# Optimization experiments

Measured on AMD Instinct MI355X. Metric: run time of the kernel, lower is better.

The kernel has to match this reference:

```python
import jax, jax.numpy as jnp
import numpy as np
from jax import lax

B, T, P, I, H = 1024, 100, 50, 96, 1024  # batch, seq_dim, pred_dim, input_dim, hidden_dim


def _gru_cell(x, h, Wih, Whh, bih, bhh):
    # PyTorch GRU gate math. Wih:[3H,in], Whh:[3H,H]
    gi = x @ Wih.T + bih
    gh = h @ Whh.T + bhh
    ir, iz, i_n = jnp.split(gi, 3, axis=-1)
    hr, hz, h_n = jnp.split(gh, 3, axis=-1)
    r = jax.nn.sigmoid(ir + hr)
    z = jax.nn.sigmoid(iz + hz)
    n = jnp.tanh(i_n + r * h_n)
    return (1.0 - z) * n + z * h


def setup_inputs() -> dict:
    key = jax.random.key(0)
    ks = jax.random.split(key, 24)
    s = 1.0 / np.sqrt(H)

    def rn(k, shape):
        return jax.random.normal(k, shape, jnp.float32) * s

    inp = {"x": jax.random.normal(ks[0], (B, T, I), jnp.float32)}
    # encoder nn.GRU: layer 0 input I, layer 1 input H
    inp["enc_Wih0"] = rn(ks[1], (3 * H, I)); inp["enc_Whh0"] = rn(ks[2], (3 * H, H))
    inp["enc_bih0"] = rn(ks[3], (3 * H,));   inp["enc_bhh0"] = rn(ks[4], (3 * H,))
    inp["enc_Wih1"] = rn(ks[5], (3 * H, H)); inp["enc_Whh1"] = rn(ks[6], (3 * H, H))
    inp["enc_bih1"] = rn(ks[7], (3 * H,));   inp["enc_bhh1"] = rn(ks[8], (3 * H,))
    # decoder GRUCells (hidden->hidden)
    inp["dec_Wih0"] = rn(ks[9], (3 * H, H)); inp["dec_Whh0"] = rn(ks[10], (3 * H, H))
    inp["dec_bih0"] = rn(ks[11], (3 * H,));  inp["dec_bhh0"] = rn(ks[12], (3 * H,))
    inp["dec_Wih1"] = rn(ks[13], (3 * H, H)); inp["dec_Whh1"] = rn(ks[14], (3 * H, H))
    inp["dec_bih1"] = rn(ks[15], (3 * H,));  inp["dec_bhh1"] = rn(ks[16], (3 * H,))
    # fc_in: I->H, fc_out: H->I
    inp["fc_in_w"] = rn(ks[17], (H, I)); inp["fc_in_b"] = rn(ks[18], (H,))
    inp["fc_out_w"] = rn(ks[19], (I, H)); inp["fc_out_b"] = rn(ks[20], (I,))
    return inp


def reference(x, enc_Wih0, enc_Whh0, enc_bih0, enc_bhh0,
              enc_Wih1, enc_Whh1, enc_bih1, enc_bhh1,
              dec_Wih0, dec_Whh0, dec_bih0, dec_bhh0,
              dec_Wih1, dec_Whh1, dec_bih1, dec_bhh1,
              fc_in_w, fc_in_b, fc_out_w, fc_out_b):
    b = x.shape[0]
    h0 = jnp.zeros((b, H), x.dtype)
    xs = jnp.transpose(x[:, :P, :], (1, 0, 2))  # [P, B, I]

    def enc0(h, xt):
        h2 = _gru_cell(xt, h, enc_Wih0, enc_Whh0, enc_bih0, enc_bhh0)
        return h2, h2

    h_enc0, seq0 = lax.scan(enc0, h0, xs)

    def enc1(h, xt):
        h2 = _gru_cell(xt, h, enc_Wih1, enc_Whh1, enc_bih1, enc_bhh1)
        return h2, h2

    h_enc1, _ = lax.scan(enc1, h0, seq0)

    def dec_step(carry, _):
        frame, hd0, hd1 = carry
        y = frame @ fc_in_w.T + fc_in_b
        hd0 = _gru_cell(y, hd0, dec_Wih0, dec_Whh0, dec_bih0, dec_bhh0)
        hd1 = _gru_cell(hd0, hd1, dec_Wih1, dec_Whh1, dec_bih1, dec_bhh1)
        frame = hd1 @ fc_out_w.T + fc_out_b + frame
        return (frame, hd0, hd1), frame

    init = (x[:, P - 1, :], h_enc0, h_enc1)
    _, outs = lax.scan(dec_step, init, None, length=T - P)  # [T-P, B, I]
    out = jnp.concatenate([x[:, :P, :], jnp.transpose(outs, (1, 0, 2))], axis=1)
    return out
```

## Files before the change

### kernel.cpp

```cpp
#include <hip/hip_runtime.h>
#include <hip/hip_bf16.h>
#include <stdint.h>

#define Bsz 1024
#define Tt  100
#define Pp  50
#define Ii  96
#define Hh  1024
#define H3  3072

typedef __bf16 bf16x8 __attribute__((ext_vector_type(8)));
typedef float f32x4 __attribute__((ext_vector_type(4)));
typedef __hip_bfloat16 bf16;

__device__ __forceinline__ void llds16(const void* g, void* l) {
    __builtin_amdgcn_global_load_lds(
        (const __attribute__((address_space(1))) void*)g,
        (__attribute__((address_space(3))) void*)l,
        16, 0, 0);
}

__device__ __forceinline__ void swz_decomp(int& bx, int& by, int& bz) {
    int gx = gridDim.x, gy = gridDim.y, gz = gridDim.z;
    int flat = blockIdx.x + gx * (blockIdx.y + gy * blockIdx.z);
    int tot = gx * gy * gz;
    if (!(tot & 7)) {
        int q = tot >> 3;
        flat = (flat & 7) * q + (flat >> 3);
    }
    bx = flat % gx;
    int rest = flat / gx;
    by = rest % gy;
    bz = rest / gy;
}

__global__ void wdesc_k(unsigned long long* slot, const void* A, const void* W,
                        const void* b, void* C, int K, int lda) {
    if (threadIdx.x == 0) {
        slot[0] = (unsigned long long)A;
        slot[1] = (unsigned long long)W;
        slot[2] = (unsigned long long)b;
        slot[3] = (unsigned long long)C;
        slot[4] = (unsigned long long)K;
        slot[5] = (unsigned long long)lda;
    }
}

__global__ void __launch_bounds__(256)
gemm_tab(const unsigned long long* __restrict__ tab, int base, int ndesc,
         const bf16* __restrict__ extraA)
{
    __shared__ bf16 As[128 * 32];
    __shared__ bf16 Ws[128 * 32];
    int flat = blockIdx.x;
    const int tot = ndesc * 192;
    if (!(tot & 7)) {
        int q = tot >> 3;
        flat = (flat & 7) * q + (flat >> 3);
    }
    const int g = flat / 192;
    const int local = flat - g * 192;
    const unsigned long long* dp = tab + (size_t)(base + g) * 8;
    const bf16* A = (const bf16*)dp[0];
    const bf16* W = (const bf16*)dp[1];
    const float* bias = (const float*)dp[2];
    float* C = (float*)dp[3];
    const int K = (int)dp[4];
    const int lda = (int)dp[5];
    if (!A) A = extraA;

    const int tn = (local % 24) * 128;
    const int tm = (local / 24) * 128;

    const int tid = threadIdx.x;
    const int lane = tid & 63;
    const int wid = tid >> 6;
    const int wr = (wid >> 1) * 64;
    const int wc = (wid & 1) * 64;
    const int srow = tid >> 2;
    const int skb = (tid & 3) * 8;

    f32x4 acc[4][4] = {};

    const bf16* ga = A + (size_t)(tm + srow) * lda + skb;
    const bf16* gw = W + (size_t)(tn + srow) * K + skb;
    bf16* lA = &As[srow * 32 + skb];
    bf16* lW = &Ws[srow * 32 + skb];
    const int nk = K >> 5;

    for (int kt = 0; kt < nk; ++kt) {
        llds16(ga, lA);
        llds16(ga + (size_t)64 * lda, lA + 64 * 32);
        llds16(gw, lW);
        llds16(gw + (size_t)64 * K, lW + 64 * 32);
        ga += 32; gw += 32;
        __syncthreads();

        const int fr = lane & 15;
        const int kg = (lane >> 4) * 8;
        bf16x8 af[4], wf[4];
#pragma unroll
        for (int i = 0; i < 4; ++i) {
            af[i] = *(const bf16x8*)&As[(wr + i * 16 + fr) * 32 + kg];
            wf[i] = *(const bf16x8*)&Ws[(wc + i * 16 + fr) * 32 + kg];
        }
#pragma unroll
        for (int mi = 0; mi < 4; ++mi)
#pragma unroll
            for (int ni = 0; ni < 4; ++ni)
                acc[mi][ni] = __builtin_amdgcn_mfma_f32_16x16x32_bf16(
                    af[mi], wf[ni], acc[mi][ni], 0, 0, 0);
        __syncthreads();
    }

    const int fr = lane & 15;
    const int fq = (lane >> 4) * 4;
#pragma unroll
    for (int mi = 0; mi < 4; ++mi)
#pragma unroll
        for (int ni = 0; ni < 4; ++ni) {
            const int col = tn + wc + ni * 16 + fr;
            const float bv = bias[col];
#pragma unroll
            for (int r = 0; r < 4; ++r) {
                const int row = tm + wr + mi * 16 + fq + r;
                C[(size_t)row * H3 + col] = acc[mi][ni][r] + bv;
            }
        }
}

template <bool OUT_BF16>
__global__ void __launch_bounds__(256)
gemm64(const bf16* __restrict__ A, const bf16* __restrict__ W,
       const float* __restrict__ bias, void* __restrict__ Cout,
       int M, int Nreal, int Ktot, int Ks, int lda, int ldc)
{
    __shared__ bf16 As[64 * 32];
    __shared__ bf16 Ws[64 * 32];
    int bx, by, bz;
    swz_decomp(bx, by, bz);
    const int s = bz;
    const float* bs = (s == 0) ? bias : nullptr;
    const int tid = threadIdx.x;
    const int lane = tid & 63;
    const int wid = tid >> 6;
    const int wr = (wid >> 1) * 32;
    const int wc = (wid & 1) * 32;
    const int tm = by * 64;
    const int tn = bx * 64;
    const int srow = tid >> 2;
    const int skb = (tid & 3) * 8;
    const int k0 = s * Ks;

    f32x4 acc[2][2] = {};

    const bf16* ga = A + (size_t)(tm + srow) * lda + k0 + skb;
    const bf16* gw = W + (size_t)(tn + srow) * Ktot + k0 + skb;
    bf16* lA = &As[srow * 32 + skb];
    bf16* lW = &Ws[srow * 32 + skb];
    const int nk = Ks >> 5;

    for (int kt = 0; kt < nk; ++kt) {
        llds16(ga, lA);
        llds16(gw, lW);
        ga += 32; gw += 32;
        __syncthreads();
        const int fr = lane & 15;
        const int kg = (lane >> 4) * 8;
        bf16x8 af[2], wf[2];
#pragma unroll
        for (int i = 0; i < 2; ++i) {
            af[i] = *(const bf16x8*)&As[(wr + i * 16 + fr) * 32 + kg];
            wf[i] = *(const bf16x8*)&Ws[(wc + i * 16 + fr) * 32 + kg];
        }
#pragma unroll
        for (int mi = 0; mi < 2; ++mi)
#pragma unroll
            for (int ni = 0; ni < 2; ++ni)
                acc[mi][ni] = __builtin_amdgcn_mfma_f32_16x16x32_bf16(
                    af[mi], wf[ni], acc[mi][ni], 0, 0, 0);
        __syncthreads();
    }

    float* Cf = (float*)Cout + (size_t)s * M * ldc;
    const int fr = lane & 15;
    const int fq = (lane >> 4) * 4;
#pragma unroll
    for (int mi = 0; mi < 2; ++mi)
#pragma unroll
        for (int ni = 0; ni < 2; ++ni) {
            const int col = tn + wc + ni * 16 + fr;
            if (col < Nreal) {
                const float bv = bs ? bs[col] : 0.f;
#pragma unroll
                for (int r = 0; r < 4; ++r) {
                    const int row = tm + wr + mi * 16 + fq + r;
                    const float v = acc[mi][ni][r] + bv;
                    if constexpr (OUT_BF16)
                        ((bf16*)Cout)[(size_t)row * ldc + col] = __float2bfloat16(v);
                    else
                        Cf[(size_t)row * ldc + col] = v;
                }
            }
        }
}

__global__ void cvt_k(const float* __restrict__ s, bf16* __restrict__ d, int n) {
    int i = blockIdx.x * blockDim.x + threadIdx.x;
    if (i < n) d[i] = __float2bfloat16(s[i]);
}

__global__ void tpose_k(const float* __restrict__ x, bf16* __restrict__ d) {
    int o = blockIdx.x * blockDim.x + threadIdx.x;
    if (o >= Tt * Bsz * Ii) return;
    int i = o % Ii;
    int b = (o / Ii) % Bsz;
    int t = o / (Ii * Bsz);
    d[o] = __float2bfloat16(x[((size_t)b * Tt + t) * Ii + i]);
}

__global__ void tposeFcin_k(const float* __restrict__ w, bf16* __restrict__ d) {
    int o = blockIdx.x * blockDim.x + threadIdx.x;
    if (o >= 128 * Hh) return;
    int r = o >> 10;
    int c = o & (Hh - 1);
    float v = (r < Ii) ? w[(size_t)c * Ii + r] : 0.f;
    d[o] = __float2bfloat16(v);
}

__global__ void __launch_bounds__(256)
bcomb_k(const float* __restrict__ W, const float* __restrict__ v,
        const float* __restrict__ b2, float* __restrict__ o) {
    __shared__ float red[256];
    int n = blockIdx.x;
    float s = 0.f;
    for (int k = threadIdx.x; k < Hh; k += 256)
        s += W[(size_t)n * Hh + k] * v[k];
    red[threadIdx.x] = s;
    __syncthreads();
    for (int w = 128; w > 0; w >>= 1) {
        if (threadIdx.x < w) red[threadIdx.x] += red[threadIdx.x + w];
        __syncthreads();
    }
    if (threadIdx.x == 0) o[n] = red[0] + b2[n];
}

__global__ void prefix_k(const float* __restrict__ x, float* __restrict__ out) {
    int idx = blockIdx.x * blockDim.x + threadIdx.x;
    if (idx >= Bsz * Pp * Ii) return;
    int b = idx / (Pp * Ii);
    int r = idx % (Pp * Ii);
    out[(size_t)b * Tt * Ii + r] = x[(size_t)b * Tt * Ii + r];
}

__global__ void finit_k(const float* __restrict__ x, float* __restrict__ fr,
                        bf16* __restrict__ frb) {
    int idx = blockIdx.x * blockDim.x + threadIdx.x;
    if (idx >= Bsz * Ii) return;
    int b = idx / Ii;
    int i = idx % Ii;
    float v = x[(size_t)b * Tt * Ii + (Pp - 1) * Ii + i];
    fr[idx] = v;
    frb[idx] = __float2bfloat16(v);
}

__global__ void __launch_bounds__(256)
gru_cell_k(const float* __restrict__ giA, const float* __restrict__ giB,
           const float* __restrict__ ghA, const float* __restrict__ ghB,
           float* __restrict__ h, bf16* __restrict__ hb) {
    int idx = blockIdx.x * 256 + threadIdx.x;
    int b = idx >> 8;
    int j = (idx & 255) << 2;
    size_t base = (size_t)b * H3 + j;
    f32x4 ir = *(const f32x4*)(giA + base);
    f32x4 iz = *(const f32x4*)(giA + base + Hh);
    f32x4 in = *(const f32x4*)(giA + base + 2 * Hh);
    if (giB) {
        ir += *(const f32x4*)(giB + base);
        iz += *(const f32x4*)(giB + base + Hh);
        in += *(const f32x4*)(giB + base + 2 * Hh);
    }
    f32x4 hr = *(const f32x4*)(ghA + base);
    f32x4 hz = *(const f32x4*)(ghA + base + Hh);
    f32x4 hn = *(const f32x4*)(ghA + base + 2 * Hh);
    if (ghB) {
        hr += *(const f32x4*)(ghB + base);
        hz += *(const f32x4*)(ghB + base + Hh);
        hn += *(const f32x4*)(ghB + base + 2 * Hh);
    }
    size_t hoff = (size_t)b * Hh + j;
    f32x4 hold = *(const f32x4*)(h + hoff);
    f32x4 hv;
    ushort4 up;
    unsigned short* us = &up.x;
#pragma unroll
    for (int e = 0; e < 4; ++e) {
        float r = 1.f / (1.f + __expf(-(ir[e] + hr[e])));
        float z = 1.f / (1.f + __expf(-(iz[e] + hz[e])));
        float n = tanhf(in[e] + r * hn[e]);
        float v = (1.f - z) * n + z * hold[e];
        hv[e] = v;
        bf16 bv = __float2bfloat16(v);
        us[e] = *(unsigned short*)&bv;
    }
    *(f32x4*)(h + hoff) = hv;
    *(ushort4*)((unsigned short*)hb + hoff) = up;
}

__global__ void __launch_bounds__(256)
frame_upd_k(const float* __restrict__ gp, float* __restrict__ frame,
            bf16* __restrict__ frameb, float* __restrict__ out_t) {
    int idx = blockIdx.x * 256 + threadIdx.x;
    if (idx >= Bsz * (Ii / 4)) return;
    int b = idx / (Ii / 4);
    int c = (idx % (Ii / 4)) * 4;
    size_t o = (size_t)b * Ii + c;
    f32x4 sum = {};
#pragma unroll
    for (int p = 0; p < 8; ++p)
        sum += *(const f32x4*)(gp + (size_t)p * Bsz * Ii + o);
    f32x4 v = *(const f32x4*)(frame + o) + sum;
    *(f32x4*)(frame + o) = v;
    ushort4 up;
    unsigned short* us = &up.x;
#pragma unroll
    for (int e = 0; e < 4; ++e) {
        bf16 bv = __float2bfloat16(v[e]);
        us[e] = *(unsigned short*)&bv;
    }
    *(ushort4*)((unsigned short*)frameb + o) = up;
    *(f32x4*)(out_t + (size_t)b * Tt * Ii + c) = v;
}

extern "C" void kernel_launch(void* const* d_in, const int* in_sizes, int n_in,
                              void* d_out, int out_size, void* d_ws, size_t ws_size,
                              hipStream_t stream) {
    const float* x      = (const float*)d_in[0];
    const float* eWih0  = (const float*)d_in[1];
    const float* eWhh0  = (const float*)d_in[2];
    const float* ebih0  = (const float*)d_in[3];
    const float* ebhh0  = (const float*)d_in[4];
    const float* eWih1  = (const float*)d_in[5];
    const float* eWhh1  = (const float*)d_in[6];
    const float* ebih1  = (const float*)d_in[7];
    const float* ebhh1  = (const float*)d_in[8];
    const float* dWih0  = (const float*)d_in[9];
    const float* dWhh0  = (const float*)d_in[10];
    const float* dbih0  = (const float*)d_in[11];
    const float* dbhh0  = (const float*)d_in[12];
    const float* dWih1  = (const float*)d_in[13];
    const float* dWhh1  = (const float*)d_in[14];
    const float* dbih1  = (const float*)d_in[15];
    const float* dbhh1  = (const float*)d_in[16];
    const float* fcin_w = (const float*)d_in[17];
    const float* fcin_b = (const float*)d_in[18];
    const float* fcout_w= (const float*)d_in[19];
    const float* fcout_b= (const float*)d_in[20];
    float* out = (float*)d_out;

    char* base = (char*)d_ws;
    size_t off = 0;
    auto alloc = [&](size_t bytes) -> void* {
        void* r = base + off;
        off += (bytes + 255) & ~(size_t)255;
        return r;
    };
    bf16* wWih0e = (bf16*)alloc((size_t)H3 * Ii * 2);
    bf16* wWhh0e = (bf16*)alloc((size_t)H3 * Hh * 2);
    bf16* wWih1e = (bf16*)alloc((size_t)H3 * Hh * 2);
    bf16* wWhh1e = (bf16*)alloc((size_t)H3 * Hh * 2);
    bf16* wWih0d = (bf16*)alloc((size_t)H3 * Hh * 2);
    bf16* wWhh0d = (bf16*)alloc((size_t)H3 * Hh * 2);
    bf16* wWih1d = (bf16*)alloc((size_t)H3 * Hh * 2);
    bf16* wWhh1d = (bf16*)alloc((size_t)H3 * Hh * 2);
    bf16* fcinT  = (bf16*)alloc((size_t)128 * Hh * 2);
    bf16* wWcomb = (bf16*)alloc((size_t)H3 * Ii * 2);
    float* bcomb = (float*)alloc((size_t)H3 * 4);
    bf16* wfcout = (bf16*)alloc((size_t)128 * Hh * 2);
    float* zbias = (float*)alloc((size_t)128 * 4);
    bf16* xbT    = (bf16*)alloc((size_t)Tt * Bsz * Ii * 2);
    float* gi1_p = (float*)alloc((size_t)Bsz * H3 * 4);
    float* gh1_p = (float*)alloc((size_t)Bsz * H3 * 4);
    float* gh0_p = (float*)alloc((size_t)Bsz * H3 * 4);
    float* gi0_p = (float*)alloc((size_t)Bsz * H3 * 4);
    float* h0    = (float*)alloc((size_t)Bsz * Hh * 4);
    float* h1    = (float*)alloc((size_t)Bsz * Hh * 4);
    bf16* h0b    = (bf16*)alloc((size_t)Bsz * Hh * 2);
    bf16* h1b    = (bf16*)alloc((size_t)Bsz * Hh * 2);
    float* gfc   = (float*)alloc((size_t)8 * Bsz * Ii * 4);
    float* frame = (float*)alloc((size_t)Bsz * Ii * 4);
    bf16* frameb = (bf16*)alloc((size_t)Bsz * Ii * 2);
    unsigned long long* tab = (unsigned long long*)alloc(8 * 8 * 8);
    if (off > ws_size) return;

    auto cvt = [&](const float* s, bf16* d, int n) {
        cvt_k<<<dim3((n + 255) / 256), dim3(256), 0, stream>>>(s, d, n);
    };
    cvt(eWih0, wWih0e, H3 * Ii);
    cvt(eWhh0, wWhh0e, H3 * Hh);
    cvt(eWih1, wWih1e, H3 * Hh);
    cvt(eWhh1, wWhh1e, H3 * Hh);
    cvt(dWih0, wWih0d, H3 * Hh);
    cvt(dWhh0, wWhh0d, H3 * Hh);
    cvt(dWih1, wWih1d, H3 * Hh);
    cvt(dWhh1, wWhh1d, H3 * Hh);
    (void)hipMemsetAsync(wfcout, 0, (size_t)128 * Hh * 2, stream);
    (void)hipMemsetAsync(zbias, 0, (size_t)128 * 4, stream);
    cvt(fcout_w, wfcout, Ii * Hh);
    tposeFcin_k<<<dim3((128 * Hh + 255) / 256), dim3(256), 0, stream>>>(fcin_w, fcinT);
    gemm64<true><<<dim3(2, 48, 1), dim3(256), 0, stream>>>(
        wWih0d, fcinT, zbias, (void*)wWcomb, H3, Ii, Hh, Hh, Hh, Ii);
    bcomb_k<<<dim3(H3), dim3(256), 0, stream>>>(dWih0, fcin_b, dbih0, bcomb);

    tpose_k<<<dim3((Tt * Bsz * Ii + 255) / 256), dim3(256), 0, stream>>>(x, xbT);
    prefix_k<<<dim3((Bsz * Pp * Ii + 255) / 256), dim3(256), 0, stream>>>(x, out);
    finit_k<<<dim3((Bsz * Ii + 255) / 256), dim3(256), 0, stream>>>(x, frame, frameb);
    (void)hipMemsetAsync(h0, 0, (size_t)Bsz * Hh * 4, stream);
    (void)hipMemsetAsync(h1, 0, (size_t)Bsz * Hh * 4, stream);
    (void)hipMemsetAsync(h0b, 0, (size_t)Bsz * Hh * 2, stream);
    (void)hipMemsetAsync(h1b, 0, (size_t)Bsz * Hh * 2, stream);

    wdesc_k<<<1, 64, 0, stream>>>(tab + 0 * 8, h0b, wWih1e, ebih1, gi1_p, Hh, Hh);
    wdesc_k<<<1, 64, 0, stream>>>(tab + 1 * 8, h1b, wWhh1e, ebhh1, gh1_p, Hh, Hh);
    wdesc_k<<<1, 64, 0, stream>>>(tab + 2 * 8, h0b, wWhh0e, ebhh0, gh0_p, Hh, Hh);
    wdesc_k<<<1, 64, 0, stream>>>(tab + 3 * 8, nullptr, wWih0e, ebih0, gi0_p, Ii, Ii);
    wdesc_k<<<1, 64, 0, stream>>>(tab + 4 * 8, h0b, wWih1d, dbih1, gi1_p, Hh, Hh);
    wdesc_k<<<1, 64, 0, stream>>>(tab + 5 * 8, h1b, wWhh1d, dbhh1, gh1_p, Hh, Hh);
    wdesc_k<<<1, 64, 0, stream>>>(tab + 6 * 8, h0b, wWhh0d, dbhh0, gh0_p, Hh, Hh);
    wdesc_k<<<1, 64, 0, stream>>>(tab + 7 * 8, frameb, wWcomb, bcomb, gi0_p, Ii, Ii);

    gemm_tab<<<dim3(384), dim3(256), 0, stream>>>(tab, 2, 2, xbT);
    gru_cell_k<<<dim3(1024), dim3(256), 0, stream>>>(
        gi0_p, nullptr, gh0_p, nullptr, h0, h0b);
    for (int i = 0; i < Pp; ++i) {
        if (i < Pp - 1) {
            gemm_tab<<<dim3(768), dim3(256), 0, stream>>>(
                tab, 0, 4, xbT + (size_t)(i + 1) * Bsz * Ii);
            gru_cell_k<<<dim3(1024), dim3(256), 0, stream>>>(
                gi1_p, nullptr, gh1_p, nullptr, h1, h1b);
            gru_cell_k<<<dim3(1024), dim3(256), 0, stream>>>(
                gi0_p, nullptr, gh0_p, nullptr, h0, h0b);
        } else {
            gemm_tab<<<dim3(384), dim3(256), 0, stream>>>(tab, 0, 2, xbT);
            gru_cell_k<<<dim3(1024), dim3(256), 0, stream>>>(
                gi1_p, nullptr, gh1_p, nullptr, h1, h1b);
        }
    }

    gemm_tab<<<dim3(384), dim3(256), 0, stream>>>(tab, 6, 2, xbT);
    gru_cell_k<<<dim3(1024), dim3(256), 0, stream>>>(
        gi0_p, nullptr, gh0_p, nullptr, h0, h0b);
    for (int t = 0; t < Tt - Pp; ++t) {
        const bool last = (t == Tt - Pp - 1);
        if (!last) {
            gemm_tab<<<dim3(576), dim3(256), 0, stream>>>(tab, 4, 3, xbT);
        } else {
            gemm_tab<<<dim3(384), dim3(256), 0, stream>>>(tab, 4, 2, xbT);
        }
        gru_cell_k<<<dim3(1024), dim3(256), 0, stream>>>(
            gi1_p, nullptr, gh1_p, nullptr, h1, h1b);
        gemm64<false><<<dim3(2, 16, 8), dim3(256), 0, stream>>>(
            h1b, wfcout, fcout_b, (void*)gfc, Bsz, Ii, Hh, Hh / 8, Hh, Ii);
        frame_upd_k<<<dim3((Bsz * (Ii / 4) + 255) / 256), dim3(256), 0, stream>>>(
            gfc, frame, frameb, out + (size_t)(Pp + t) * Ii);
        if (!last) {
            gemm_tab<<<dim3(192), dim3(256), 0, stream>>>(tab, 7, 1, xbT);
            gru_cell_k<<<dim3(1024), dim3(256), 0, stream>>>(
                gi0_p, nullptr, gh0_p, nullptr, h0, h0b);
        }
    }
}
```

Baseline: 5.952 ms.

## Use 64-wide K tiles with XOR-swizzled LDS, pad input dim, merge GRU cell launches

The table-driven GEMM now stages 64-element K slices per iteration instead of 32. It uses an XOR swizzle on the LDS chunk index to avoid bank conflicts, which halves the number of barrier pairs per K loop. Because the input-dimension operands (x, Wih0, Wcomb, frame) are no longer a multiple of 64, they are zero-padded from 96 to 128 columns. The two encoder GRU cell updates per step are merged into one 2048-block launch to save a kernel launch per timestep. The cost is doubled LDS per block, a little extra padded work on the small-K GEMMs, and possible occupancy pressure.

```diff
diff --git a/kernel.cpp b/kernel.cpp
--- a/kernel.cpp
+++ b/kernel.cpp
@@ -50,8 +50,8 @@
 gemm_tab(const unsigned long long* __restrict__ tab, int base, int ndesc,
          const bf16* __restrict__ extraA)
 {
-    __shared__ bf16 As[128 * 32];
-    __shared__ bf16 Ws[128 * 32];
+    __shared__ bf16 As[128 * 64];
+    __shared__ bf16 Ws[128 * 64];
     int flat = blockIdx.x;
     const int tot = ndesc * 192;
     if (!(tot & 7)) {
@@ -77,44 +77,49 @@
     const int wid = tid >> 6;
     const int wr = (wid >> 1) * 64;
     const int wc = (wid & 1) * 64;
-    const int srow = tid >> 2;
-    const int skb = (tid & 3) * 8;
+    const int srow = tid >> 3;
+    const int schk = ((tid & 7) ^ (srow & 7)) * 8;
+    const int sdst = tid * 16;
+    const int fr = lane & 15;
+    const int hi = lane >> 4;
 
     f32x4 acc[4][4] = {};
 
-    const bf16* ga = A + (size_t)(tm + srow) * lda + skb;
-    const bf16* gw = W + (size_t)(tn + srow) * K + skb;
-    bf16* lA = &As[srow * 32 + skb];
-    bf16* lW = &Ws[srow * 32 + skb];
-    const int nk = K >> 5;
+    const bf16* ga = A + (size_t)(tm + srow) * lda + schk;
+    const bf16* gw = W + (size_t)(tn + srow) * K + schk;
+    char* lA = (char*)As + sdst;
+    char* lW = (char*)Ws + sdst;
+    const int nk = K >> 6;
 
     for (int kt = 0; kt < nk; ++kt) {
-        llds16(ga, lA);
-        llds16(ga + (size_t)64 * lda, lA + 64 * 32);
-        llds16(gw, lW);
-        llds16(gw + (size_t)64 * K, lW + 64 * 32);
-        ga += 32; gw += 32;
+#pragma unroll
+        for (int m = 0; m < 4; ++m) {
+            llds16(ga + (size_t)(32 * m) * lda, lA + 32 * m * 128);
+            llds16(gw + (size_t)(32 * m) * K,  lW + 32 * m * 128);
+        }
+        ga += 64; gw += 64;
         __syncthreads();
 
-        const int fr = lane & 15;
-        const int kg = (lane >> 4) * 8;
-        bf16x8 af[4], wf[4];
-#pragma unroll
-        for (int i = 0; i < 4; ++i) {
-            af[i] = *(const bf16x8*)&As[(wr + i * 16 + fr) * 32 + kg];
-            wf[i] = *(const bf16x8*)&Ws[(wc + i * 16 + fr) * 32 + kg];
-        }
-#pragma unroll
-        for (int mi = 0; mi < 4; ++mi)
-#pragma unroll
-            for (int ni = 0; ni < 4; ++ni)
-                acc[mi][ni] = __builtin_amdgcn_mfma_f32_16x16x32_bf16(
-                    af[mi], wf[ni], acc[mi][ni], 0, 0, 0);
+#pragma unroll
+        for (int kk = 0; kk < 2; ++kk) {
+            bf16x8 af[4], wf[4];
+            const int chk = (((kk << 2) + hi) ^ (fr & 7)) * 8;
+#pragma unroll
+            for (int i = 0; i < 4; ++i) {
+                af[i] = *(const bf16x8*)&As[(wr + i * 16 + fr) * 64 + chk];
+                wf[i] = *(const bf16x8*)&Ws[(wc + i * 16 + fr) * 64 + chk];
+            }
+#pragma unroll
+            for (int mi = 0; mi < 4; ++mi)
+#pragma unroll
+                for (int ni = 0; ni < 4; ++ni)
+                    acc[mi][ni] = __builtin_amdgcn_mfma_f32_16x16x32_bf16(
+                        af[mi], wf[ni], acc[mi][ni], 0, 0, 0);
+        }
         __syncthreads();
     }
 
-    const int fr = lane & 15;
-    const int fq = (lane >> 4) * 4;
+    const int fq = hi * 4;
 #pragma unroll
     for (int mi = 0; mi < 4; ++mi)
 #pragma unroll
@@ -210,13 +215,20 @@
     if (i < n) d[i] = __float2bfloat16(s[i]);
 }
 
+__global__ void cvtpad_k(const float* __restrict__ s, bf16* __restrict__ d, int n) {
+    int o = blockIdx.x * blockDim.x + threadIdx.x;
+    if (o >= n * 128) return;
+    int r = o >> 7, c = o & 127;
+    d[o] = __float2bfloat16(c < Ii ? s[(size_t)r * Ii + c] : 0.f);
+}
+
 __global__ void tpose_k(const float* __restrict__ x, bf16* __restrict__ d) {
     int o = blockIdx.x * blockDim.x + threadIdx.x;
-    if (o >= Tt * Bsz * Ii) return;
-    int i = o % Ii;
-    int b = (o / Ii) % Bsz;
-    int t = o / (Ii * Bsz);
-    d[o] = __float2bfloat16(x[((size_t)b * Tt + t) * Ii + i]);
+    if (o >= Tt * Bsz * 128) return;
+    int i = o & 127;
+    int b = (o >> 7) & (Bsz - 1);
+    int t = o >> 17;
+    d[o] = __float2bfloat16(i < Ii ? x[((size_t)b * Tt + t) * Ii + i] : 0.f);
 }
 
 __global__ void tposeFcin_k(const float* __restrict__ w, bf16* __restrict__ d) {
@@ -261,50 +273,62 @@
     int i = idx % Ii;
     float v = x[(size_t)b * Tt * Ii + (Pp - 1) * Ii + i];
     fr[idx] = v;
-    frb[idx] = __float2bfloat16(v);
-}
-
-__global__ void __launch_bounds__(256)
-gru_cell_k(const float* __restrict__ giA, const float* __restrict__ giB,
-           const float* __restrict__ ghA, const float* __restrict__ ghB,
+    frb[(size_t)b * 128 + i] = __float2bfloat16(v);
+}
+
+#define CELL_BODY(IDX, GI, GH, H, HB)                                        \
+    {                                                                        \
+        int b_ = (IDX) >> 8;                                                 \
+        int j_ = ((IDX) & 255) << 2;                                         \
+        size_t base_ = (size_t)b_ * H3 + j_;                                 \
+        f32x4 ir = *(const f32x4*)((GI) + base_);                            \
+        f32x4 iz = *(const f32x4*)((GI) + base_ + Hh);                       \
+        f32x4 in = *(const f32x4*)((GI) + base_ + 2 * Hh);                   \
+        f32x4 hr = *(const f32x4*)((GH) + base_);                            \
+        f32x4 hz = *(const f32x4*)((GH) + base_ + Hh);                       \
+        f32x4 hn = *(const f32x4*)((GH) + base_ + 2 * Hh);                   \
+        size_t hoff_ = (size_t)b_ * Hh + j_;                                 \
+        f32x4 hold = *(const f32x4*)((H) + hoff_);                           \
+        f32x4 hv;                                                            \
+        ushort4 up;                                                          \
+        unsigned short* us = &up.x;                                          \
+        _Pragma("unroll")                                                    \
+        for (int e = 0; e < 4; ++e) {                                        \
+            float r = 1.f / (1.f + __expf(-(ir[e] + hr[e])));                \
+            float z = 1.f / (1.f + __expf(-(iz[e] + hz[e])));                \
+            float n = tanhf(in[e] + r * hn[e]);                              \
+            float v = (1.f - z) * n + z * hold[e];                           \
+            hv[e] = v;                                                       \
+            bf16 bv = __float2bfloat16(v);                                   \
+            us[e] = *(unsigned short*)&bv;                                   \
+        }                                                                    \
+        *(f32x4*)((H) + hoff_) = hv;                                         \
+        *(ushort4*)((unsigned short*)(HB) + hoff_) = up;                     \
+    }
+
+__global__ void __launch_bounds__(256)
+gru_cell_k(const float* __restrict__ gi, const float* __restrict__ gh,
            float* __restrict__ h, bf16* __restrict__ hb) {
     int idx = blockIdx.x * 256 + threadIdx.x;
-    int b = idx >> 8;
-    int j = (idx & 255) << 2;
-    size_t base = (size_t)b * H3 + j;
-    f32x4 ir = *(const f32x4*)(giA + base);
-    f32x4 iz = *(const f32x4*)(giA + base + Hh);
-    f32x4 in = *(const f32x4*)(giA + base + 2 * Hh);
-    if (giB) {
-        ir += *(const f32x4*)(giB + base);
-        iz += *(const f32x4*)(giB + base + Hh);
-        in += *(const f32x4*)(giB + base + 2 * Hh);
-    }
-    f32x4 hr = *(const f32x4*)(ghA + base);
-    f32x4 hz = *(const f32x4*)(ghA + base + Hh);
-    f32x4 hn = *(const f32x4*)(ghA + base + 2 * Hh);
-    if (ghB) {
-        hr += *(const f32x4*)(ghB + base);
-        hz += *(const f32x4*)(ghB + base + Hh);
-        hn += *(const f32x4*)(ghB + base + 2 * Hh);
-    }
-    size_t hoff = (size_t)b * Hh + j;
-    f32x4 hold = *(const f32x4*)(h + hoff);
-    f32x4 hv;
-    ushort4 up;
-    unsigned short* us = &up.x;
-#pragma unroll
-    for (int e = 0; e < 4; ++e) {
-        float r = 1.f / (1.f + __expf(-(ir[e] + hr[e])));
-        float z = 1.f / (1.f + __expf(-(iz[e] + hz[e])));
-        float n = tanhf(in[e] + r * hn[e]);
-        float v = (1.f - z) * n + z * hold[e];
-        hv[e] = v;
-        bf16 bv = __float2bfloat16(v);
-        us[e] = *(unsigned short*)&bv;
-    }
-    *(f32x4*)(h + hoff) = hv;
-    *(ushort4*)((unsigned short*)hb + hoff) = up;
+    CELL_BODY(idx, gi, gh, h, hb);
+}
+
+__global__ void __launch_bounds__(256)
+gru_cell2_k(const float* __restrict__ giA, const float* __restrict__ ghA,
+            float* __restrict__ hA, bf16* __restrict__ hbA,
+            const float* __restrict__ giB, const float* __restrict__ ghB,
+            float* __restrict__ hB, bf16* __restrict__ hbB) {
+    int bid = blockIdx.x;
+    const float* gi = giA;
+    const float* gh = ghA;
+    float* h = hA;
+    bf16* hb = hbA;
+    if (bid >= 1024) {
+        gi = giB; gh = ghB; h = hB; hb = hbB;
+        bid -= 1024;
+    }
+    int idx = bid * 256 + threadIdx.x;
+    CELL_BODY(idx, gi, gh, h, hb);
 }
 
 __global__ void __launch_bounds__(256)
@@ -328,7 +352,7 @@
         bf16 bv = __float2bfloat16(v[e]);
         us[e] = *(unsigned short*)&bv;
     }
-    *(ushort4*)((unsigned short*)frameb + o) = up;
+    *(ushort4*)((unsigned short*)frameb + (size_t)b * 128 + c) = up;
     *(f32x4*)(out_t + (size_t)b * Tt * Ii + c) = v;
 }
 
@@ -365,20 +389,20 @@
         off += (bytes + 255) & ~(size_t)255;
         return r;
     };
-    bf16* wWih0e = (bf16*)alloc((size_t)H3 * Ii * 2);
+    bf16* wWih0e = (bf16*)alloc((size_t)H3 * 128 * 2);
     bf16* wWhh0e = (bf16*)alloc((size_t)H3 * Hh * 2);
     bf16* wWih1e = (bf16*)alloc((size_t)H3 * Hh * 2);
     bf16* wWhh1e = (bf16*)alloc((size_t)H3 * Hh * 2);
-    bf16* wWih0d = (bf16*)alloc((size_t)H3 * Hh * 2);
     bf16* wWhh0d = (bf16*)alloc((size_t)H3 * Hh * 2);
     bf16* wWih1d = (bf16*)alloc((size_t)H3 * Hh * 2);
     bf16* wWhh1d = (bf16*)alloc((size_t)H3 * Hh * 2);
+    bf16* wWih0d = (bf16*)alloc((size_t)H3 * Hh * 2);
     bf16* fcinT  = (bf16*)alloc((size_t)128 * Hh * 2);
-    bf16* wWcomb = (bf16*)alloc((size_t)H3 * Ii * 2);
+    bf16* wWcomb = (bf16*)alloc((size_t)H3 * 128 * 2);
     float* bcomb = (float*)alloc((size_t)H3 * 4);
     bf16* wfcout = (bf16*)alloc((size_t)128 * Hh * 2);
     float* zbias = (float*)alloc((size_t)128 * 4);
-    bf16* xbT    = (bf16*)alloc((size_t)Tt * Bsz * Ii * 2);
+    bf16* xbT    = (bf16*)alloc((size_t)Tt * Bsz * 128 * 2);
     float* gi1_p = (float*)alloc((size_t)Bsz * H3 * 4);
     float* gh1_p = (float*)alloc((size_t)Bsz * H3 * 4);
     float* gh0_p = (float*)alloc((size_t)Bsz * H3 * 4);
@@ -389,14 +413,14 @@
     bf16* h1b    = (bf16*)alloc((size_t)Bsz * Hh * 2);
     float* gfc   = (float*)alloc((size_t)8 * Bsz * Ii * 4);
     float* frame = (float*)alloc((size_t)Bsz * Ii * 4);
-    bf16* frameb = (bf16*)alloc((size_t)Bsz * Ii * 2);
+    bf16* frameb = (bf16*)alloc((size_t)Bsz * 128 * 2);
     unsigned long long* tab = (unsigned long long*)alloc(8 * 8 * 8);
     if (off > ws_size) return;
 
     auto cvt = [&](const float* s, bf16* d, int n) {
         cvt_k<<<dim3((n + 255) / 256), dim3(256), 0, stream>>>(s, d, n);
     };
-    cvt(eWih0, wWih0e, H3 * Ii);
+    cvtpad_k<<<dim3((H3 * 128 + 255) / 256), dim3(256), 0, stream>>>(eWih0, wWih0e, H3);
     cvt(eWhh0, wWhh0e, H3 * Hh);
     cvt(eWih1, wWih1e, H3 * Hh);
     cvt(eWhh1, wWhh1e, H3 * Hh);
@@ -405,14 +429,16 @@
     cvt(dWih1, wWih1d, H3 * Hh);
     cvt(dWhh1, wWhh1d, H3 * Hh);
     (void)hipMemsetAsync(wfcout, 0, (size_t)128 * Hh * 2, stream);
+    (void)hipMemsetAsync(wWcomb, 0, (size_t)H3 * 128 * 2, stream);
     (void)hipMemsetAsync(zbias, 0, (size_t)128 * 4, stream);
+    (void)hipMemsetAsync(frameb, 0, (size_t)Bsz * 128 * 2, stream);
     cvt(fcout_w, wfcout, Ii * Hh);
     tposeFcin_k<<<dim3((128 * Hh + 255) / 256), dim3(256), 0, stream>>>(fcin_w, fcinT);
     gemm64<true><<<dim3(2, 48, 1), dim3(256), 0, stream>>>(
-        wWih0d, fcinT, zbias, (void*)wWcomb, H3, Ii, Hh, Hh, Hh, Ii);
+        wWih0d, fcinT, zbias, (void*)wWcomb, H3, Ii, Hh, Hh, Hh, 128);
     bcomb_k<<<dim3(H3), dim3(256), 0, stream>>>(dWih0, fcin_b, dbih0, bcomb);
 
-    tpose_k<<<dim3((Tt * Bsz * Ii + 255) / 256), dim3(256), 0, stream>>>(x, xbT);
+    tpose_k<<<dim3((Tt * Bsz * 128 + 255) / 256), dim3(256), 0, stream>>>(x, xbT);
     prefix_k<<<dim3((Bsz * Pp * Ii + 255) / 256), dim3(256), 0, stream>>>(x, out);
     finit_k<<<dim3((Bsz * Ii + 255) / 256), dim3(256), 0, stream>>>(x, frame, frameb);
     (void)hipMemsetAsync(h0, 0, (size_t)Bsz * Hh * 4, stream);
@@ -423,33 +449,28 @@
     wdesc_k<<<1, 64, 0, stream>>>(tab + 0 * 8, h0b, wWih1e, ebih1, gi1_p, Hh, Hh);
     wdesc_k<<<1, 64, 0, stream>>>(tab + 1 * 8, h1b, wWhh1e, ebhh1, gh1_p, Hh, Hh);
     wdesc_k<<<1, 64, 0, stream>>>(tab + 2 * 8, h0b, wWhh0e, ebhh0, gh0_p, Hh, Hh);
-    wdesc_k<<<1, 64, 0, stream>>>(tab + 3 * 8, nullptr, wWih0e, ebih0, gi0_p, Ii, Ii);
+    wdesc_k<<<1, 64, 0, stream>>>(tab + 3 * 8, nullptr, wWih0e, ebih0, gi0_p, 128, 128);
     wdesc_k<<<1, 64, 0, stream>>>(tab + 4 * 8, h0b, wWih1d, dbih1, gi1_p, Hh, Hh);
     wdesc_k<<<1, 64, 0, stream>>>(tab + 5 * 8, h1b, wWhh1d, dbhh1, gh1_p, Hh, Hh);
     wdesc_k<<<1, 64, 0, stream>>>(tab + 6 * 8, h0b, wWhh0d, dbhh0, gh0_p, Hh, Hh);
-    wdesc_k<<<1, 64, 0, stream>>>(tab + 7 * 8, frameb, wWcomb, bcomb, gi0_p, Ii, Ii);
+    wdesc_k<<<1, 64, 0, stream>>>(tab + 7 * 8, frameb, wWcomb, bcomb, gi0_p, 128, 128);
 
     gemm_tab<<<dim3(384), dim3(256), 0, stream>>>(tab, 2, 2, xbT);
-    gru_cell_k<<<dim3(1024), dim3(256), 0, stream>>>(
-        gi0_p, nullptr, gh0_p, nullptr, h0, h0b);
+    gru_cell_k<<<dim3(1024), dim3(256), 0, stream>>>(gi0_p, gh0_p, h0, h0b);
     for (int i = 0; i < Pp; ++i) {
         if (i < Pp - 1) {
             gemm_tab<<<dim3(768), dim3(256), 0, stream>>>(
-                tab, 0, 4, xbT + (size_t)(i + 1) * Bsz * Ii);
-            gru_cell_k<<<dim3(1024), dim3(256), 0, stream>>>(
-                gi1_p, nullptr, gh1_p, nullptr, h1, h1b);
-            gru_cell_k<<<dim3(1024), dim3(256), 0, stream>>>(
-                gi0_p, nullptr, gh0_p, nullptr, h0, h0b);
+                tab, 0, 4, xbT + (size_t)(i + 1) * Bsz * 128);
+            gru_cell2_k<<<dim3(2048), dim3(256), 0, stream>>>(
+                gi1_p, gh1_p, h1, h1b, gi0_p, gh0_p, h0, h0b);
         } else {
             gemm_tab<<<dim3(384), dim3(256), 0, stream>>>(tab, 0, 2, xbT);
-            gru_cell_k<<<dim3(1024), dim3(256), 0, stream>>>(
-                gi1_p, nullptr, gh1_p, nullptr, h1, h1b);
+            gru_cell_k<<<dim3(1024), dim3(256), 0, stream>>>(gi1_p, gh1_p, h1, h1b);
         }
     }
 
     gemm_tab<<<dim3(384), dim3(256), 0, stream>>>(tab, 6, 2, xbT);
-    gru_cell_k<<<dim3(1024), dim3(256), 0, stream>>>(
-        gi0_p, nullptr, gh0_p, nullptr, h0, h0b);
+    gru_cell_k<<<dim3(1024), dim3(256), 0, stream>>>(gi0_p, gh0_p, h0, h0b);
     for (int t = 0; t < Tt - Pp; ++t) {
         const bool last = (t == Tt - Pp - 1);
         if (!last) {
@@ -457,16 +478,14 @@
         } else {
             gemm_tab<<<dim3(384), dim3(256), 0, stream>>>(tab, 4, 2, xbT);
         }
-        gru_cell_k<<<dim3(1024), dim3(256), 0, stream>>>(
-            gi1_p, nullptr, gh1_p, nullptr, h1, h1b);
+        gru_cell_k<<<dim3(1024), dim3(256), 0, stream>>>(gi1_p, gh1_p, h1, h1b);
         gemm64<false><<<dim3(2, 16, 8), dim3(256), 0, stream>>>(
             h1b, wfcout, fcout_b, (void*)gfc, Bsz, Ii, Hh, Hh / 8, Hh, Ii);
         frame_upd_k<<<dim3((Bsz * (Ii / 4) + 255) / 256), dim3(256), 0, stream>>>(
             gfc, frame, frameb, out + (size_t)(Pp + t) * Ii);
         if (!last) {
             gemm_tab<<<dim3(192), dim3(256), 0, stream>>>(tab, 7, 1, xbT);
-            gru_cell_k<<<dim3(1024), dim3(256), 0, stream>>>(
-                gi0_p, nullptr, gh0_p, nullptr, h0, h0b);
-        }
-    }
-}
+            gru_cell_k<<<dim3(1024), dim3(256), 0, stream>>>(gi0_p, gh0_p, h0, h0b);
+        }
+    }
+}
```

Result: faster. 5.481 ms (-7.9%).
